# Kernel optimization log

Measured on AMD Instinct MI355X. Metric: run time of the kernel, lower is better.

## Reference

```python
import jax, jax.numpy as jnp
import numpy as np

D_MODEL = 1024
N_HEAD = 16
HEAD_DIM = D_MODEL // N_HEAD
BATCH = 2
SEQ = 2048


def setup_inputs() -> dict:
    key = jax.random.key(0)
    ks = jax.random.split(key, 5)
    std = np.sqrt(2.0 / (D_MODEL + D_MODEL)).astype(np.float32)
    return {
        "in_features": jax.random.normal(ks[0], (BATCH, SEQ, D_MODEL), dtype=jnp.float32),
        "Wq": jax.random.normal(ks[1], (D_MODEL, D_MODEL), dtype=jnp.float32) * std,
        "Wk": jax.random.normal(ks[2], (D_MODEL, D_MODEL), dtype=jnp.float32) * std,
        "Wv": jax.random.normal(ks[3], (D_MODEL, D_MODEL), dtype=jnp.float32) * std,
        "Wo": jax.random.normal(ks[4], (D_MODEL, D_MODEL), dtype=jnp.float32) * std,
    }


def reference(in_features, Wq, Wk, Wv, Wo):
    B, S, _ = in_features.shape
    # projections: x @ W (custom Linear stores weight as [in, out], no bias)
    q = (in_features @ Wq).reshape(B, S, N_HEAD, HEAD_DIM).transpose(0, 2, 1, 3)  # [B,H,S,Dh]
    k = (in_features @ Wk).reshape(B, S, N_HEAD, HEAD_DIM).transpose(0, 2, 1, 3)
    v = (in_features @ Wv).reshape(B, S, N_HEAD, HEAD_DIM).transpose(0, 2, 1, 3)
    scale = HEAD_DIM ** (-0.5)
    scores = jnp.einsum("bhqd,bhkd->bhqk", q, k) * scale  # [B,H,S,S]
    causal = jnp.tril(jnp.ones((S, S), dtype=bool))
    scores = jnp.where(causal, scores, -jnp.inf)
    attn = jax.nn.softmax(scores, axis=-1)
    ctx = jnp.einsum("bhqk,bhkd->bhqd", attn, v)  # [B,H,S,Dh]
    ctx = ctx.transpose(0, 2, 1, 3).reshape(B, S, D_MODEL)
    return ctx @ Wo
```

## Files before the change

### kernel.cpp

```cpp
#include <hip/hip_runtime.h>
#include <hip/hip_bf16.h>

#define DM 1024
#define NH 16
#define HD 64
#define B_ 2
#define S_ 2048
#define M_ (B_*S_)

typedef __attribute__((ext_vector_type(8))) short bf16x8;
typedef __attribute__((ext_vector_type(4))) float f32x4;

__device__ __forceinline__ float bf2f(ushort u) {
  union { unsigned u32; float f; } c; c.u32 = ((unsigned)u) << 16; return c.f;
}
__device__ __forceinline__ ushort f2bf(float f) {
  union { float f; unsigned u32; } c; c.f = f;
  unsigned u = c.u32;
  unsigned r = (u + 0x7fffu + ((u >> 16) & 1u)) >> 16;
  return (ushort)r;
}

__global__ void cvt_x(const float* __restrict__ x, ushort* __restrict__ xb) {
  int i = blockIdx.x * blockDim.x + threadIdx.x;
  float4 v = ((const float4*)x)[i];
  ushort4 o;
  o.x = f2bf(v.x); o.y = f2bf(v.y); o.z = f2bf(v.z); o.w = f2bf(v.w);
  ((ushort4*)xb)[i] = o;
}

__global__ void cvt_transpose_w(const float* __restrict__ W0, const float* __restrict__ W1,
                                const float* __restrict__ W2, const float* __restrict__ W3,
                                ushort* __restrict__ wt) {
  __shared__ float tile[64][65];
  int z = blockIdx.z;
  const float* W = (z == 0) ? W0 : (z == 1) ? W1 : (z == 2) ? W2 : W3;
  ushort* Wt = wt + (size_t)z * (DM * DM);
  int tx = threadIdx.x, ty = threadIdx.y;
  int c0 = blockIdx.x * 64, r0 = blockIdx.y * 64;
  #pragma unroll
  for (int i = ty; i < 64; i += 4) tile[i][tx] = W[(size_t)(r0 + i) * DM + c0 + tx];
  __syncthreads();
  #pragma unroll
  for (int i = ty; i < 64; i += 4) Wt[(size_t)(c0 + i) * DM + r0 + tx] = f2bf(tile[tx][i]);
}

template <int MODE>
__device__ __forceinline__ void gemm_body(const ushort* __restrict__ A,
                                          const ushort* __restrict__ Bt,
                                          ushort* __restrict__ Cb,
                                          float* __restrict__ Cf) {
  __shared__ __align__(16) ushort As[128 * 40];
  __shared__ __align__(16) ushort Bs[128 * 40];
  const int K = DM;
  int m0 = blockIdx.y * 128;
  int n0 = blockIdx.x * 128;
  int t = threadIdx.x;
  int lane = t & 63, wave = t >> 6;
  int wm = (wave >> 1) * 64, wn = (wave & 1) * 64;
  int lrow = lane & 15, quad = lane >> 4;

  f32x4 acc[4][4];
  #pragma unroll
  for (int r = 0; r < 4; ++r)
    #pragma unroll
    for (int c = 0; c < 4; ++c) acc[r][c] = (f32x4){0.f, 0.f, 0.f, 0.f};

  for (int k0 = 0; k0 < K; k0 += 32) {
    #pragma unroll
    for (int cch = 0; cch < 2; ++cch) {
      int ch = t + cch * 256;
      int row = ch >> 2, cc = ch & 3;
      *(uint4*)(As + row * 40 + cc * 8) =
          *(const uint4*)(A + (size_t)(m0 + row) * K + k0 + cc * 8);
      *(uint4*)(Bs + row * 40 + cc * 8) =
          *(const uint4*)(Bt + (size_t)(n0 + row) * K + k0 + cc * 8);
    }
    __syncthreads();
    bf16x8 af[4], bfr[4];
    #pragma unroll
    for (int r = 0; r < 4; ++r)
      af[r] = *(const bf16x8*)(As + (wm + r * 16 + lrow) * 40 + quad * 8);
    #pragma unroll
    for (int c = 0; c < 4; ++c)
      bfr[c] = *(const bf16x8*)(Bs + (wn + c * 16 + lrow) * 40 + quad * 8);
    #pragma unroll
    for (int r = 0; r < 4; ++r)
      #pragma unroll
      for (int c = 0; c < 4; ++c)
        acc[r][c] = __builtin_amdgcn_mfma_f32_16x16x32_bf16(af[r], bfr[c], acc[r][c], 0, 0, 0);
    __syncthreads();
  }

  #pragma unroll
  for (int r = 0; r < 4; ++r) {
    #pragma unroll
    for (int c = 0; c < 4; ++c) {
      #pragma unroll
      for (int e = 0; e < 4; ++e) {
        int m = m0 + wm + r * 16 + quad * 4 + e;
        int n = n0 + wn + c * 16 + lrow;
        if (MODE == 0) {
          Cf[(size_t)m * DM + n] = acc[r][c][e];
        } else if (MODE == 1) {
          int b = m >> 11, s = m & 2047, h = n >> 6, d = n & 63;
          Cb[(((size_t)(b * NH + h)) * S_ + s) * HD + d] = f2bf(acc[r][c][e]);
        } else {
          int b = m >> 11, s = m & 2047, h = n >> 6, d = n & 63;
          Cb[(((size_t)(b * NH + h)) * HD + d) * S_ + s] = f2bf(acc[r][c][e]);
        }
      }
    }
  }
}

__global__ __launch_bounds__(256, 2) void gemm_qkv(const ushort* __restrict__ A,
                                                   const ushort* __restrict__ wt,
                                                   ushort* __restrict__ qkv) {
  int z = blockIdx.z;
  if (z < 2)
    gemm_body<1>(A, wt + (size_t)z * (DM * DM), qkv + (size_t)z * ((size_t)M_ * DM), nullptr);
  else
    gemm_body<2>(A, wt + (size_t)z * (DM * DM), qkv + (size_t)z * ((size_t)M_ * DM), nullptr);
}

__global__ __launch_bounds__(256, 2) void gemm_out(const ushort* __restrict__ A,
                                                   const ushort* __restrict__ wt,
                                                   float* __restrict__ C) {
  gemm_body<0>(A, wt, nullptr, C);
}

struct AttnState {
  f32x4 o[4];
  float l[4];
};

__device__ __forceinline__ void attn_tile_compute(
    int q0, int kt, bf16x8 qf0, bf16x8 qf1,
    const bf16x8 kf0[4], const bf16x8 kf1[4],
    const bf16x8 vf0[4], const bf16x8 vf1[4],
    ushort* pl, AttnState& st, int lrow, int quad) {
  f32x4 s[4];
  #pragma unroll
  for (int c = 0; c < 4; ++c) {
    f32x4 z = (f32x4){0.f, 0.f, 0.f, 0.f};
    z = __builtin_amdgcn_mfma_f32_16x16x32_bf16(qf0, kf0[c], z, 0, 0, 0);
    z = __builtin_amdgcn_mfma_f32_16x16x32_bf16(qf1, kf1[c], z, 0, 0, 0);
    s[c] = z;
  }
  #pragma unroll
  for (int e = 0; e < 4; ++e) {
    int q = q0 + quad * 4 + e;
    #pragma unroll
    for (int c = 0; c < 4; ++c) {
      int key = kt + c * 16 + lrow;
      float pv = __expf(s[c][e] * 0.125f);
      pv = (key <= q) ? pv : 0.f;
      st.l[e] += pv;
      pl[(quad * 4 + e) * 72 + c * 16 + lrow] = f2bf(pv);
    }
  }
  bf16x8 pf0 = *(const bf16x8*)(pl + lrow * 72 + quad * 8);
  bf16x8 pf1 = *(const bf16x8*)(pl + lrow * 72 + 32 + quad * 8);
  #pragma unroll
  for (int dt = 0; dt < 4; ++dt) {
    st.o[dt] = __builtin_amdgcn_mfma_f32_16x16x32_bf16(pf0, vf0[dt], st.o[dt], 0, 0, 0);
    st.o[dt] = __builtin_amdgcn_mfma_f32_16x16x32_bf16(pf1, vf1[dt], st.o[dt], 0, 0, 0);
  }
}

__global__ __launch_bounds__(256, 2) void attn_mfma(const ushort* __restrict__ Q,
                                                    const ushort* __restrict__ Kmat,
                                                    const ushort* __restrict__ Vt,
                                                    ushort* __restrict__ ctx) {
  __shared__ __align__(16) ushort Ks[2][64 * 72];
  __shared__ __align__(16) ushort Vs[2][64 * 72];
  __shared__ __align__(16) ushort plds[4][16 * 72];
  int t = threadIdx.x;
  int lane = t & 63, wave = t >> 6;
  int lrow = lane & 15, quad = lane >> 4;
  int bh = blockIdx.y;
  int p = blockIdx.x;
  int qt_lo = p, qt_hi = 31 - p;
  const ushort* Kb = Kmat + (size_t)bh * S_ * HD;
  const ushort* Vb = Vt + (size_t)bh * HD * S_;
  ushort* pl = plds[wave];
  int b = bh >> 4, h = bh & 15;

  int r0 = t >> 3, s0 = (t & 7) * 8;
  int r1 = (t + 256) >> 3, s1 = s0;

  int q0_lo = qt_lo * 64 + wave * 16;
  int q0_hi = qt_hi * 64 + wave * 16;
  const ushort* Qlo = Q + ((size_t)bh * S_ + q0_lo) * HD;
  const ushort* Qhi = Q + ((size_t)bh * S_ + q0_hi) * HD;
  bf16x8 qlo0 = *(const bf16x8*)(Qlo + (size_t)lrow * HD + quad * 8);
  bf16x8 qlo1 = *(const bf16x8*)(Qlo + (size_t)lrow * HD + 32 + quad * 8);
  bf16x8 qhi0 = *(const bf16x8*)(Qhi + (size_t)lrow * HD + quad * 8);
  bf16x8 qhi1 = *(const bf16x8*)(Qhi + (size_t)lrow * HD + 32 + quad * 8);

  AttnState lo, hi;
  #pragma unroll
  for (int i = 0; i < 4; ++i) {
    lo.o[i] = (f32x4){0.f, 0.f, 0.f, 0.f}; hi.o[i] = (f32x4){0.f, 0.f, 0.f, 0.f};
    lo.l[i] = 0.f; hi.l[i] = 0.f;
  }

  int kend = qt_hi * 64;

  {
    uint4 ka = *(const uint4*)(Kb + (size_t)r0 * HD + s0);
    uint4 kb2 = *(const uint4*)(Kb + (size_t)r1 * HD + s1);
    uint4 va = *(const uint4*)(Vb + (size_t)r0 * S_ + s0);
    uint4 vb2 = *(const uint4*)(Vb + (size_t)r1 * S_ + s1);
    *(uint4*)(Ks[0] + r0 * 72 + s0) = ka;
    *(uint4*)(Ks[0] + r1 * 72 + s1) = kb2;
    *(uint4*)(Vs[0] + r0 * 72 + s0) = va;
    *(uint4*)(Vs[0] + r1 * 72 + s1) = vb2;
  }
  __syncthreads();

  for (int kt = 0; kt <= kend; kt += 64) {
    int cur = (kt >> 6) & 1, nxt = cur ^ 1;
    bool has_next = (kt < kend);

    uint4 ka, kb2, va, vb2;
    if (has_next) {
      int ktn = kt + 64;
      ka  = *(const uint4*)(Kb + (size_t)(ktn + r0) * HD + s0);
      kb2 = *(const uint4*)(Kb + (size_t)(ktn + r1) * HD + s1);
      va  = *(const uint4*)(Vb + (size_t)r0 * S_ + ktn + s0);
      vb2 = *(const uint4*)(Vb + (size_t)r1 * S_ + ktn + s1);
    }

    bf16x8 kf0[4], kf1[4], vf0[4], vf1[4];
    #pragma unroll
    for (int c = 0; c < 4; ++c) {
      const ushort* kr = Ks[cur] + (c * 16 + lrow) * 72;
      kf0[c] = *(const bf16x8*)(kr + quad * 8);
      kf1[c] = *(const bf16x8*)(kr + 32 + quad * 8);
      const ushort* vr = Vs[cur] + (c * 16 + lrow) * 72;
      vf0[c] = *(const bf16x8*)(vr + quad * 8);
      vf1[c] = *(const bf16x8*)(vr + 32 + quad * 8);
    }

    attn_tile_compute(q0_hi, kt, qhi0, qhi1, kf0, kf1, vf0, vf1, pl, hi, lrow, quad);
    if (kt <= qt_lo * 64)
      attn_tile_compute(q0_lo, kt, qlo0, qlo1, kf0, kf1, vf0, vf1, pl, lo, lrow, quad);

    if (has_next) {
      *(uint4*)(Ks[nxt] + r0 * 72 + s0) = ka;
      *(uint4*)(Ks[nxt] + r1 * 72 + s1) = kb2;
      *(uint4*)(Vs[nxt] + r0 * 72 + s0) = va;
      *(uint4*)(Vs[nxt] + r1 * 72 + s1) = vb2;
    }
    __syncthreads();
  }

  #pragma unroll
  for (int half = 0; half < 2; ++half) {
    AttnState& st = half ? hi : lo;
    int q0 = half ? q0_hi : q0_lo;
    #pragma unroll
    for (int e = 0; e < 4; ++e) {
      float l = st.l[e];
      l += __shfl_xor(l, 1);
      l += __shfl_xor(l, 2);
      l += __shfl_xor(l, 4);
      l += __shfl_xor(l, 8);
      float rinv = 1.0f / l;
      int q = q0 + quad * 4 + e;
      #pragma unroll
      for (int dt = 0; dt < 4; ++dt)
        ctx[((size_t)b * S_ + q) * DM + h * HD + dt * 16 + lrow] = f2bf(st.o[dt][e] * rinv);
    }
  }
}

extern "C" void kernel_launch(void* const* d_in, const int* in_sizes, int n_in,
                              void* d_out, int out_size, void* d_ws, size_t ws_size,
                              hipStream_t stream) {
  const float* x  = (const float*)d_in[0];
  const float* Wq = (const float*)d_in[1];
  const float* Wk = (const float*)d_in[2];
  const float* Wv = (const float*)d_in[3];
  const float* Wo = (const float*)d_in[4];
  float* out = (float*)d_out;
  ushort* ws = (ushort*)d_ws;

  ushort* xb  = ws;
  ushort* wt  = xb + (size_t)M_ * DM;
  ushort* qkv = wt + (size_t)4 * DM * DM;
  ushort* ctx = qkv + (size_t)3 * M_ * DM;

  cvt_x<<<dim3((M_ * DM) / 4 / 256), 256, 0, stream>>>(x, xb);
  cvt_transpose_w<<<dim3(16, 16, 4), dim3(64, 4), 0, stream>>>(Wq, Wk, Wv, Wo, wt);
  gemm_qkv<<<dim3(DM / 128, M_ / 128, 3), 256, 0, stream>>>(xb, wt, qkv);
  attn_mfma<<<dim3(16, B_ * NH), 256, 0, stream>>>(qkv, qkv + (size_t)M_ * DM,
                                                   qkv + (size_t)2 * M_ * DM, ctx);
  gemm_out<<<dim3(DM / 128, M_ / 128), 256, 0, stream>>>(ctx, wt + (size_t)3 * DM * DM, out);
}
```

Before: 204.6 us.

## Use direct global-to-LDS loads in GEMM and transposed score layout in attention

Measured after the change: 189.7 us. 7.3% less time.

```diff
diff --git a/kernel.cpp b/kernel.cpp
--- a/kernel.cpp
+++ b/kernel.cpp
@@ -19,6 +19,14 @@
   unsigned u = c.u32;
   unsigned r = (u + 0x7fffu + ((u >> 16) & 1u)) >> 16;
   return (ushort)r;
+}
+__device__ __forceinline__ unsigned fbits(float f) {
+  union { float f; unsigned u; } c; c.f = f; return c.u;
+}
+
+__device__ __forceinline__ void async16(const ushort* g, ushort* l) {
+  __builtin_amdgcn_global_load_lds((const __attribute__((address_space(1))) void*)g,
+                                   (__attribute__((address_space(3))) void*)l, 16, 0, 0);
 }
 
 __global__ void cvt_x(const float* __restrict__ x, ushort* __restrict__ xb) {
@@ -50,8 +58,8 @@
                                           const ushort* __restrict__ Bt,
                                           ushort* __restrict__ Cb,
                                           float* __restrict__ Cf) {
-  __shared__ __align__(16) ushort As[128 * 40];
-  __shared__ __align__(16) ushort Bs[128 * 40];
+  __shared__ __align__(16) ushort As[128 * 32];
+  __shared__ __align__(16) ushort Bs[128 * 32];
   const int K = DM;
   int m0 = blockIdx.y * 128;
   int n0 = blockIdx.x * 128;
@@ -60,6 +68,9 @@
   int wm = (wave >> 1) * 64, wn = (wave & 1) * 64;
   int lrow = lane & 15, quad = lane >> 4;
 
+  int Ra = wave * 32;
+  int srow = lane >> 2, scol = (lane & 3) * 8;
+
   f32x4 acc[4][4];
   #pragma unroll
   for (int r = 0; r < 4; ++r)
@@ -67,23 +78,21 @@
     for (int c = 0; c < 4; ++c) acc[r][c] = (f32x4){0.f, 0.f, 0.f, 0.f};
 
   for (int k0 = 0; k0 < K; k0 += 32) {
-    #pragma unroll
-    for (int cch = 0; cch < 2; ++cch) {
-      int ch = t + cch * 256;
-      int row = ch >> 2, cc = ch & 3;
-      *(uint4*)(As + row * 40 + cc * 8) =
-          *(const uint4*)(A + (size_t)(m0 + row) * K + k0 + cc * 8);
-      *(uint4*)(Bs + row * 40 + cc * 8) =
-          *(const uint4*)(Bt + (size_t)(n0 + row) * K + k0 + cc * 8);
-    }
+    const ushort* ga = A + (size_t)(m0 + Ra + srow) * K + k0 + scol;
+    const ushort* gb = Bt + (size_t)(n0 + Ra + srow) * K + k0 + scol;
+    async16(ga,            As + Ra * 32);
+    async16(ga + 16 * K,   As + (Ra + 16) * 32);
+    async16(gb,            Bs + Ra * 32);
+    async16(gb + 16 * K,   Bs + (Ra + 16) * 32);
     __syncthreads();
+
     bf16x8 af[4], bfr[4];
     #pragma unroll
     for (int r = 0; r < 4; ++r)
-      af[r] = *(const bf16x8*)(As + (wm + r * 16 + lrow) * 40 + quad * 8);
+      af[r] = *(const bf16x8*)(As + (wm + r * 16 + lrow) * 32 + quad * 8);
     #pragma unroll
     for (int c = 0; c < 4; ++c)
-      bfr[c] = *(const bf16x8*)(Bs + (wn + c * 16 + lrow) * 40 + quad * 8);
+      bfr[c] = *(const bf16x8*)(Bs + (wn + c * 16 + lrow) * 32 + quad * 8);
     #pragma unroll
     for (int r = 0; r < 4; ++r)
       #pragma unroll
@@ -132,7 +141,7 @@
 
 struct AttnState {
   f32x4 o[4];
-  float l[4];
+  float l;
 };
 
 __device__ __forceinline__ void attn_tile_compute(
@@ -144,21 +153,26 @@
   #pragma unroll
   for (int c = 0; c < 4; ++c) {
     f32x4 z = (f32x4){0.f, 0.f, 0.f, 0.f};
-    z = __builtin_amdgcn_mfma_f32_16x16x32_bf16(qf0, kf0[c], z, 0, 0, 0);
-    z = __builtin_amdgcn_mfma_f32_16x16x32_bf16(qf1, kf1[c], z, 0, 0, 0);
+    z = __builtin_amdgcn_mfma_f32_16x16x32_bf16(kf0[c], qf0, z, 0, 0, 0);
+    z = __builtin_amdgcn_mfma_f32_16x16x32_bf16(kf1[c], qf1, z, 0, 0, 0);
     s[c] = z;
   }
-  #pragma unroll
-  for (int e = 0; e < 4; ++e) {
-    int q = q0 + quad * 4 + e;
-    #pragma unroll
-    for (int c = 0; c < 4; ++c) {
-      int key = kt + c * 16 + lrow;
-      float pv = __expf(s[c][e] * 0.125f);
-      pv = (key <= q) ? pv : 0.f;
-      st.l[e] += pv;
-      pl[(quad * 4 + e) * 72 + c * 16 + lrow] = f2bf(pv);
-    }
+  int q = q0 + lrow;
+  #pragma unroll
+  for (int c = 0; c < 4; ++c) {
+    float pv[4];
+    #pragma unroll
+    for (int e = 0; e < 4; ++e) {
+      int key = kt + c * 16 + quad * 4 + e;
+      float v = __expf(s[c][e] * 0.125f);
+      v = (key <= q) ? v : 0.f;
+      pv[e] = v;
+      st.l += v;
+    }
+    uint2 pk;
+    pk.x = __builtin_amdgcn_perm(fbits(pv[1]), fbits(pv[0]), 0x07060302u);
+    pk.y = __builtin_amdgcn_perm(fbits(pv[3]), fbits(pv[2]), 0x07060302u);
+    *(uint2*)(pl + lrow * 72 + c * 16 + quad * 4) = pk;
   }
   bf16x8 pf0 = *(const bf16x8*)(pl + lrow * 72 + quad * 8);
   bf16x8 pf1 = *(const bf16x8*)(pl + lrow * 72 + 32 + quad * 8);
@@ -203,8 +217,8 @@
   #pragma unroll
   for (int i = 0; i < 4; ++i) {
     lo.o[i] = (f32x4){0.f, 0.f, 0.f, 0.f}; hi.o[i] = (f32x4){0.f, 0.f, 0.f, 0.f};
-    lo.l[i] = 0.f; hi.l[i] = 0.f;
-  }
+  }
+  lo.l = 0.f; hi.l = 0.f;
 
   int kend = qt_hi * 64;
 
@@ -261,14 +275,13 @@
   for (int half = 0; half < 2; ++half) {
     AttnState& st = half ? hi : lo;
     int q0 = half ? q0_hi : q0_lo;
+    float l = st.l;
+    l += __shfl_xor(l, 16);
+    l += __shfl_xor(l, 32);
+    float rl = 1.0f / l;
     #pragma unroll
     for (int e = 0; e < 4; ++e) {
-      float l = st.l[e];
-      l += __shfl_xor(l, 1);
-      l += __shfl_xor(l, 2);
-      l += __shfl_xor(l, 4);
-      l += __shfl_xor(l, 8);
-      float rinv = 1.0f / l;
+      float rinv = __shfl(rl, quad * 4 + e);
       int q = q0 + quad * 4 + e;
       #pragma unroll
       for (int dt = 0; dt < 4; ++dt)
```
